# Optimization experiments

Hardware: AMD Instinct MI355X
Metric: run time of the kernel (lower is better)

## Reference

```python
import jax, jax.numpy as jnp
import numpy as np
from jax import lax

B_, CIN, COUT, H, W = 8, 64, 64, 64, 64
DIN, DSTATE, K, DTRANK = 128, 16, 4, 4  # d_inner=2*C, d_state=16, 4 scan dirs, dt_rank=ceil(64/16)


def setup_inputs():
    key = jax.random.key(0)
    ks = jax.random.split(key, 10)
    f = lambda k, s, sc=0.02: jax.random.normal(k, s, jnp.float32) * sc
    return {
        "x": jax.random.normal(ks[0], (B_, CIN, H, W), jnp.float32),
        "conv_w": f(ks[1], (COUT, CIN, 3, 3)),
        "conv_b": jnp.zeros((COUT,), jnp.float32),
        "gn_g": jnp.ones((COUT,), jnp.float32),
        "gn_b": jnp.zeros((COUT,), jnp.float32),
        "ln1_g": jnp.ones((COUT,), jnp.float32),
        "ln1_b": jnp.zeros((COUT,), jnp.float32),
        "in_proj_w": f(ks[2], (COUT, 2 * DIN)),
        "dw_w": f(ks[3], (DIN, 1, 3, 3)),
        "dw_b": jnp.zeros((DIN,), jnp.float32),
        "x_proj_w": f(ks[4], (K, DTRANK + 2 * DSTATE, DIN)),
        "dt_w": f(ks[5], (K, DIN, DTRANK)),
        "dt_b": f(ks[6], (K, DIN), 0.01),
        "A_logs": jnp.tile(jnp.log(jnp.arange(1, DSTATE + 1, dtype=jnp.float32)), (K, DIN, 1)),
        "Ds": jnp.ones((K, DIN), jnp.float32),
        "out_norm_g": jnp.ones((DIN,), jnp.float32),
        "out_norm_b": jnp.zeros((DIN,), jnp.float32),
        "out_proj_w": f(ks[7], (DIN, COUT)),
    }


def _ln(x, g, b, eps=1e-5):
    m = x.mean(-1, keepdims=True)
    v = ((x - m) ** 2).mean(-1, keepdims=True)
    return (x - m) * lax.rsqrt(v + eps) * g + b


def reference(x, conv_w, conv_b, gn_g, gn_b, ln1_g, ln1_b, in_proj_w, dw_w, dw_b,
              x_proj_w, dt_w, dt_b, A_logs, Ds, out_norm_g, out_norm_b, out_proj_w):
    # BasicConv2d: conv3x3 (stride 1, pad 1) + GroupNorm(2) + SiLU
    y = lax.conv_general_dilated(x, conv_w, (1, 1), [(1, 1), (1, 1)],
                                 dimension_numbers=("NCHW", "OIHW", "NCHW"))
    y = y + conv_b[None, :, None, None]
    Bb, C, Hh, Ww = y.shape
    yg = y.reshape(Bb, 2, C // 2, Hh, Ww)
    m = yg.mean((2, 3, 4), keepdims=True)
    v = ((yg - m) ** 2).mean((2, 3, 4), keepdims=True)
    y = ((yg - m) * lax.rsqrt(v + 1e-5)).reshape(Bb, C, Hh, Ww)
    y = y * gn_g[None, :, None, None] + gn_b[None, :, None, None]
    y = jax.nn.silu(y)
    # VSSBlock on NHWC: LN -> SS2D -> residual
    xb = y.transpose(0, 2, 3, 1)                       # (B,H,W,C)
    h = _ln(xb, ln1_g, ln1_b)
    xz = h @ in_proj_w                                 # (B,H,W,2*DIN)
    xm, z = jnp.split(xz, 2, axis=-1)
    xm = xm.transpose(0, 3, 1, 2)                      # (B,DIN,H,W)
    xm = lax.conv_general_dilated(xm, dw_w, (1, 1), [(1, 1), (1, 1)],
                                  dimension_numbers=("NCHW", "OIHW", "NCHW"),
                                  feature_group_count=DIN)
    xm = jax.nn.silu(xm + dw_b[None, :, None, None])
    L = Hh * Ww
    x1 = xm.reshape(Bb, DIN, L)                        # HW order
    x2 = xm.transpose(0, 1, 3, 2).reshape(Bb, DIN, L)  # WH order
    xs = jnp.stack([x1, x2], 1)
    xs = jnp.concatenate([xs, jnp.flip(xs, -1)], 1)    # (B,4,DIN,L)
    xdbl = jnp.einsum("bkdl,kcd->bkcl", xs, x_proj_w)
    dts, Bs, Cs = jnp.split(xdbl, [DTRANK, DTRANK + DSTATE], axis=2)
    dts = jnp.einsum("bkrl,kdr->bkdl", dts, dt_w)
    dt = jax.nn.softplus(dts + dt_b[None, :, :, None])  # (B,4,DIN,L)
    A = -jnp.exp(A_logs)                                # (K,DIN,DSTATE)
    # selective scan over L (time-major)
    u_t = xs.transpose(3, 0, 1, 2)
    dt_t = dt.transpose(3, 0, 1, 2)
    B_t = Bs.transpose(3, 0, 1, 2)
    C_t = Cs.transpose(3, 0, 1, 2)

    def step(hst, inp):
        u, d, Bc, Cc = inp
        hst = hst * jnp.exp(d[..., None] * A) + (d * u)[..., None] * Bc[:, :, None, :]
        return hst, jnp.einsum("bkdn,bkn->bkd", hst, Cc)

    h0 = jnp.zeros((Bb, K, DIN, DSTATE), xs.dtype)
    _, ys = lax.scan(step, h0, (u_t, dt_t, B_t, C_t))  # ys: (L,B,4,DIN)
    out_y = ys.transpose(1, 2, 3, 0) + Ds[None, :, :, None] * xs
    inv_y = jnp.flip(out_y[:, 2:4], -1)
    wh_y = out_y[:, 1].reshape(Bb, DIN, Ww, Hh).transpose(0, 1, 3, 2).reshape(Bb, DIN, L)
    invwh_y = inv_y[:, 1].reshape(Bb, DIN, Ww, Hh).transpose(0, 1, 3, 2).reshape(Bb, DIN, L)
    yv = out_y[:, 0] + inv_y[:, 0] + wh_y + invwh_y    # (B,DIN,L)
    yv = yv.transpose(0, 2, 1).reshape(Bb, Hh, Ww, DIN)
    yv = _ln(yv, out_norm_g, out_norm_b)
    yv = yv * jax.nn.silu(z)
    vss = xb + yv @ out_proj_w                          # VSSBlock residual
    return vss.transpose(0, 3, 1, 2) + y                # MambaDU residual
```

## Files before the change

kernel.cpp:

```cpp
#include <hip/hip_runtime.h>
#include <hip/hip_bf16.h>

#define BD   8
#define CD   64
#define HD   64
#define WD   64
#define LD   4096
#define DINN 128
#define KDIR 4
#define NST  16
#define SUBL 32
#define L2E  1.442695040888963f

typedef const float* fp;

__device__ __forceinline__ float sigm(float x) { return 1.f / (1.f + __expf(-x)); }
__device__ __forceinline__ float softplusf(float x) {
    float e = __expf(-fabsf(x));
    return fmaxf(x, 0.f) + __logf(1.f + e);
}
__device__ __forceinline__ int pmap(int k, int l) {
    int m = (k & 2) ? (LD - 1 - l) : l;
    return (k & 1) ? (((m & 63) << 6) | (m >> 6)) : m;
}

__global__ __launch_bounds__(256) void k_conv(fp x, fp cw, fp cb, float* conv_out, float* gstats) {
    __shared__ float xt[64][3][68];
    __shared__ float red[4][4];
    int bx = blockIdx.x; int b = bx >> 6; int h = bx & 63;
    int t = threadIdx.x;
    for (int idx = t; idx < 64 * 3 * 64; idx += 256) {
        int ci = idx / 192, rem = idx % 192, r = rem >> 6, w = rem & 63;
        int hs = h + r - 1;
        float v = 0.f;
        if (hs >= 0 && hs < 64) v = x[((b * 64 + ci) * 64 + hs) * 64 + w];
        xt[ci][r][w + 1] = v;
    }
    for (int idx = t; idx < 64 * 3; idx += 256) {
        int ci = idx / 3, r = idx % 3;
        xt[ci][r][0] = 0.f; xt[ci][r][65] = 0.f; xt[ci][r][66] = 0.f; xt[ci][r][67] = 0.f;
    }
    __syncthreads();
    int co = t & 63, wq = t >> 6;
    float acc[16];
#pragma unroll
    for (int j = 0; j < 16; j++) acc[j] = 0.f;
    for (int ci = 0; ci < 64; ci++) {
        float wv[9];
        fp wp = cw + (co * 64 + ci) * 9;
#pragma unroll
        for (int q = 0; q < 9; q++) wv[q] = wp[q];
#pragma unroll
        for (int r = 0; r < 3; r++) {
            const float* row = &xt[ci][r][wq * 16];
            float xw[20];
#pragma unroll
            for (int q = 0; q < 5; q++) {
                float4 f = ((const float4*)row)[q];
                xw[4 * q] = f.x; xw[4 * q + 1] = f.y; xw[4 * q + 2] = f.z; xw[4 * q + 3] = f.w;
            }
#pragma unroll
            for (int j = 0; j < 16; j++)
                acc[j] += wv[r * 3 + 0] * xw[j] + wv[r * 3 + 1] * xw[j + 1] + wv[r * 3 + 2] * xw[j + 2];
        }
    }
    float bias = cb[co];
    __syncthreads();
    float* ot = &xt[0][0][0];
#pragma unroll
    for (int j = 0; j < 16; j++) ot[co * 64 + wq * 16 + j] = acc[j] + bias;
    __syncthreads();
    float ps0 = 0.f, pq0 = 0.f, ps1 = 0.f, pq1 = 0.f;
    for (int idx = t; idx < 4096; idx += 256) {
        int c2 = idx >> 6, w2 = idx & 63;
        float v = ot[idx];
        conv_out[((b * 64 + c2) * 64 + h) * 64 + w2] = v;
        bool g0 = c2 < 32;
        float v2 = v * v;
        ps0 += g0 ? v : 0.f; pq0 += g0 ? v2 : 0.f;
        ps1 += g0 ? 0.f : v; pq1 += g0 ? 0.f : v2;
    }
#pragma unroll
    for (int off = 32; off; off >>= 1) {
        ps0 += __shfl_xor(ps0, off); pq0 += __shfl_xor(pq0, off);
        ps1 += __shfl_xor(ps1, off); pq1 += __shfl_xor(pq1, off);
    }
    int wid = t >> 6;
    if ((t & 63) == 0) { red[wid][0] = ps0; red[wid][1] = pq0; red[wid][2] = ps1; red[wid][3] = pq1; }
    __syncthreads();
    if (t < 4) {
        float v = red[0][t] + red[1][t] + red[2][t] + red[3][t];
        atomicAdd(&gstats[b * 4 + t], v);
    }
}

__global__ __launch_bounds__(256) void k_gnapply(const float* conv_out, const float* gstats,
                                                 fp gng, fp gnb, float* y_nhwc) {
    __shared__ float tile[64][65];
    int bx = blockIdx.x; int b = bx >> 6; int p0 = (bx & 63) * 64;
    int t = threadIdx.x;
    const float invN = 1.f / (32.f * 4096.f);
    float s0 = gstats[b * 4 + 0], q0 = gstats[b * 4 + 1];
    float s1 = gstats[b * 4 + 2], q1 = gstats[b * 4 + 3];
    float m0 = s0 * invN, r0 = rsqrtf(q0 * invN - m0 * m0 + 1e-5f);
    float m1 = s1 * invN, r1 = rsqrtf(q1 * invN - m1 * m1 + 1e-5f);
    for (int idx = t; idx < 4096; idx += 256) {
        int c = idx >> 6, pi = idx & 63;
        float v = conv_out[(b * 64 + c) * LD + p0 + pi];
        float mean = (c < 32) ? m0 : m1, rstd = (c < 32) ? r0 : r1;
        v = (v - mean) * rstd * gng[c] + gnb[c];
        v = v * sigm(v);
        tile[c][pi] = v;
    }
    __syncthreads();
    for (int idx = t; idx < 4096; idx += 256) {
        int pi = idx >> 6, c = idx & 63;
        y_nhwc[(b * LD + p0 + pi) * 64 + c] = tile[c][pi];
    }
}

__global__ __launch_bounds__(256) void k_lninproj(const float* y_nhwc, fp lng, fp lnb, fp ipw,
                                                  float* xmc, float* zsil) {
    __shared__ float hn[4][64];
    int bp0 = blockIdx.x * 4;
    int t = threadIdx.x;
    int pix = t >> 6, lane = t & 63;
    {
        float v = y_nhwc[(bp0 + pix) * 64 + lane];
        float s = v, s2 = v * v;
#pragma unroll
        for (int off = 32; off; off >>= 1) { s += __shfl_xor(s, off); s2 += __shfl_xor(s2, off); }
        float mean = s * (1.f / 64.f);
        float rstd = rsqrtf(s2 * (1.f / 64.f) - mean * mean + 1e-5f);
        hn[pix][lane] = (v - mean) * rstd * lng[lane] + lnb[lane];
    }
    __syncthreads();
    float a0 = 0.f, a1 = 0.f, a2 = 0.f, a3 = 0.f;
    for (int c = 0; c < 64; c++) {
        float w = ipw[c * 256 + t];
        a0 += hn[0][c] * w; a1 += hn[1][c] * w; a2 += hn[2][c] * w; a3 += hn[3][c] * w;
    }
    float accv[4] = {a0, a1, a2, a3};
#pragma unroll
    for (int p = 0; p < 4; p++) {
        int bp = bp0 + p;
        float v = accv[p];
        if (t < 128) xmc[bp * 128 + t] = v;
        else         zsil[bp * 128 + (t - 128)] = v * sigm(v);
    }
}

__global__ __launch_bounds__(256) void k_dwconv(const float* xmc, fp dww, fp dwb, float* xm_dw) {
    int id = blockIdx.x * 256 + threadIdx.x;
    int d = id & 127, p = (id >> 7) & (LD - 1), b = id >> 19;
    int h = p >> 6, w = p & 63;
    float wv[9];
#pragma unroll
    for (int q = 0; q < 9; q++) wv[q] = dww[d * 9 + q];
    float acc = dwb[d];
#pragma unroll
    for (int i = 0; i < 3; i++) {
        int hs = h + i - 1; if (hs < 0 || hs > 63) continue;
#pragma unroll
        for (int j = 0; j < 3; j++) {
            int ws = w + j - 1; if (ws < 0 || ws > 63) continue;
            acc += xmc[((b << 12) + (hs << 6) + ws) * 128 + d] * wv[i * 3 + j];
        }
    }
    acc = acc * sigm(acc);
    xm_dw[id] = acc;
}

__global__ __launch_bounds__(192) void k_proj(const float* xm_dw, fp xpw, float* dts4, float* xBC) {
    __shared__ float u_lds[64 * 130];
    __shared__ float w_lds[128 * 40];
    int bx = blockIdx.x;
    int lt = bx & 63; int bk = bx >> 6; int k = bk & 3; int b = bk >> 2;
    int l0 = lt * 64;
    int t = threadIdx.x;
    for (int idx = t; idx < 36 * 128; idx += 192) {
        int c = idx % 36, d = idx / 36;
        w_lds[d * 40 + c] = xpw[(k * 36 + c) * 128 + d];
    }
    for (int idx = t; idx < 64 * 128; idx += 192) {
        int l = idx >> 7, d = idx & 127;
        u_lds[l * 130 + d] = xm_dw[(b * LD + pmap(k, l0 + l)) * 128 + d];
    }
    __syncthreads();
    int l = t & 63, cg = t >> 6;
    float acc[12];
#pragma unroll
    for (int i = 0; i < 12; i++) acc[i] = 0.f;
    for (int d = 0; d < 128; d++) {
        float uv = u_lds[l * 130 + d];
        const float* wr = &w_lds[d * 40 + cg * 12];
#pragma unroll
        for (int q = 0; q < 3; q++) {
            float4 f = ((const float4*)wr)[q];
            acc[4 * q + 0] += f.x * uv;
            acc[4 * q + 1] += f.y * uv;
            acc[4 * q + 2] += f.z * uv;
            acc[4 * q + 3] += f.w * uv;
        }
    }
    int base = bk * LD + l0 + l;
#pragma unroll
    for (int i = 0; i < 12; i++) {
        int c = cg * 12 + i;
        if (c < 4) dts4[base * 4 + c] = acc[i];
        else       xBC[base * 32 + (c - 4)] = acc[i];
    }
}

__global__ __launch_bounds__(256) void k_scan1(const float* xm_dw, const float* dts4, const float* xBC,
                                               fp dtw, fp dtbp, fp alog,
                                               float* Pbuf, float* Hbuf, int NCr, int CLr) {
    __shared__ float s_dt[SUBL * 128];
    __shared__ float s_b[SUBL * 16];
    __shared__ float s_d4[SUBL * 4];
    int c = blockIdx.x, k = blockIdx.y, b = blockIdx.z;
    int t = threadIdx.x; int d = t & 127; int ng = t >> 7;
    int bk = b * 4 + k;
    int kd = k * 128 + d;
    float w0 = dtw[kd * 4 + 0], w1 = dtw[kd * 4 + 1], w2 = dtw[kd * 4 + 2], w3 = dtw[kd * 4 + 3];
    float dtb = dtbp[kd];
    float base = -__expf(alog[kd * 16]) * L2E;
    float A2[8];
    bool geo = true;
#pragma unroll
    for (int n = 0; n < 8; n++) {
        A2[n] = -__expf(alog[kd * 16 + ng * 8 + n]) * L2E;
        float ideal = (float)(ng * 8 + n + 1) * base;
        geo = geo && (fabsf(A2[n] - ideal) <= 1e-4f * fabsf(ideal));
    }
    float h[8]; float sdt = 0.f;
#pragma unroll
    for (int n = 0; n < 8; n++) h[n] = 0.f;
    int l0 = c * CLr;
    for (int ss = 0; ss < CLr; ss += SUBL) {
        int ls = l0 + ss;
        const float4* gd = (const float4*)&dts4[(size_t)(bk * LD + ls) * 4];
        if (t < SUBL) ((float4*)s_d4)[t] = gd[t];
        const float4* gx = (const float4*)&xBC[(size_t)(bk * LD + ls) * 32];
        for (int i = t; i < SUBL * 4; i += 256) { int s = i >> 2, q = i & 3; ((float4*)s_b)[s * 4 + q] = gx[s * 8 + q]; }
        __syncthreads();
#pragma unroll
        for (int i = 0; i < SUBL / 2; i++) {
            int s = (t >> 7) + i * 2;
            float4 dv = ((const float4*)s_d4)[s];
            s_dt[s * 128 + d] = softplusf(dv.x * w0 + dv.y * w1 + dv.z * w2 + dv.w * w3 + dtb);
        }
        __syncthreads();
        int pbase = pmap(k, ls);
        int pstep = pmap(k, ls + 1) - pbase;
        const float* up = xm_dw + (size_t)(b * LD + pbase) * 128 + d;
        long ustep = (long)pstep * 128;
        if (geo) {
#pragma unroll 2
            for (int s = 0; s < SUBL; s++) {
                float dtv = s_dt[s * 128 + d];
                sdt += dtv;
                float r = exp2f(dtv * base);
                float u = *up; up += ustep;
                float du = dtv * u;
                const float4* Bp = (const float4*)&s_b[s * 16 + ng * 8];
                float4 B0 = Bp[0], B1 = Bp[1];
                float r2 = r * r, r3 = r2 * r, r4 = r2 * r2;
                float p5 = r4 * r, p6 = r4 * r2, p7 = r4 * r3, p8 = r4 * r4;
                float a1 = r, a2 = r2, a3 = r3, a4 = r4, a5 = p5, a6 = p6, a7 = p7, a8 = p8;
                if (ng == 1) { a1 *= p8; a2 *= p8; a3 *= p8; a4 *= p8; a5 *= p8; a6 *= p8; a7 *= p8; a8 *= p8; }
                h[0] = a1 * h[0] + du * B0.x;
                h[1] = a2 * h[1] + du * B0.y;
                h[2] = a3 * h[2] + du * B0.z;
                h[3] = a4 * h[3] + du * B0.w;
                h[4] = a5 * h[4] + du * B1.x;
                h[5] = a6 * h[5] + du * B1.y;
                h[6] = a7 * h[6] + du * B1.z;
                h[7] = a8 * h[7] + du * B1.w;
            }
        } else {
#pragma unroll 2
            for (int s = 0; s < SUBL; s++) {
                float dtv = s_dt[s * 128 + d];
                sdt += dtv;
                float u = *up; up += ustep;
                float du = dtv * u;
                const float4* Bp = (const float4*)&s_b[s * 16 + ng * 8];
                float4 B0 = Bp[0], B1 = Bp[1];
                float Bv[8] = {B0.x, B0.y, B0.z, B0.w, B1.x, B1.y, B1.z, B1.w};
#pragma unroll
                for (int n = 0; n < 8; n++) {
                    float a = exp2f(dtv * A2[n]);
                    h[n] = a * h[n] + du * Bv[n];
                }
            }
        }
        __syncthreads();
    }
    int obase = (bk * NCr + c) * 2048 + ng * 8 * 128 + d;
#pragma unroll
    for (int n = 0; n < 8; n++) {
        Pbuf[obase + n * 128] = exp2f(sdt * A2[n]);
        Hbuf[obase + n * 128] = h[n];
    }
}

__global__ __launch_bounds__(256) void k_scan2(const float* Pbuf, const float* Hbuf, float* Hinit, int NCr) {
    int id = blockIdx.x * 256 + threadIdx.x;
    int nd = id & 2047; int bk = id >> 11;
    float h = 0.f;
    int base = bk * NCr * 2048 + nd;
    for (int c = 0; c < NCr; c++) {
        int idx = base + c * 2048;
        Hinit[idx] = h;
        h = Hbuf[idx] + Pbuf[idx] * h;
    }
}

__global__ __launch_bounds__(256) void k_scan3(const float* xm_dw, const float* dts4, const float* xBC,
                                               fp dtw, fp dtbp, fp alog, fp dsp,
                                               const float* Hinit, float* yv, int NCr, int CLr) {
    __shared__ float s_dt[SUBL * 128];
    __shared__ float s_bc[SUBL * 32];
    __shared__ float s_d4[SUBL * 4];
    int c = blockIdx.x, k = blockIdx.y, b = blockIdx.z;
    int t = threadIdx.x; int d = t & 127; int ng = t >> 7;
    int bk = b * 4 + k;
    int kd = k * 128 + d;
    float w0 = dtw[kd * 4 + 0], w1 = dtw[kd * 4 + 1], w2 = dtw[kd * 4 + 2], w3 = dtw[kd * 4 + 3];
    float dtb = dtbp[kd];
    float Dv = dsp[kd];
    float base = -__expf(alog[kd * 16]) * L2E;
    float A2[8];
    bool geo = true;
#pragma unroll
    for (int n = 0; n < 8; n++) {
        A2[n] = -__expf(alog[kd * 16 + ng * 8 + n]) * L2E;
        float ideal = (float)(ng * 8 + n + 1) * base;
        geo = geo && (fabsf(A2[n] - ideal) <= 1e-4f * fabsf(ideal));
    }
    int hbase = (bk * NCr + c) * 2048 + ng * 8 * 128 + d;
    float h[8];
#pragma unroll
    for (int n = 0; n < 8; n++) h[n] = Hinit[hbase + n * 128];
    int l0 = c * CLr;
    for (int ss = 0; ss < CLr; ss += SUBL) {
        int ls = l0 + ss;
        const float4* gd = (const float4*)&dts4[(size_t)(bk * LD + ls) * 4];
        if (t < SUBL) ((float4*)s_d4)[t] = gd[t];
        const float4* gx = (const float4*)&xBC[(size_t)(bk * LD + ls) * 32];
        ((float4*)s_bc)[t] = gx[t];
        __syncthreads();
#pragma unroll
        for (int i = 0; i < SUBL / 2; i++) {
            int s = (t >> 7) + i * 2;
            float4 dv = ((const float4*)s_d4)[s];
            s_dt[s * 128 + d] = softplusf(dv.x * w0 + dv.y * w1 + dv.z * w2 + dv.w * w3 + dtb);
        }
        __syncthreads();
        int pbase = pmap(k, ls);
        int pstep = pmap(k, ls + 1) - pbase;
        const float* up = xm_dw + (size_t)(b * LD + pbase) * 128 + d;
        float* yp = yv + (size_t)(b * LD + pbase) * 128 + d;
        long ustep = (long)pstep * 128;
        if (geo) {
#pragma unroll 2
            for (int s = 0; s < SUBL; s++) {
                float dtv = s_dt[s * 128 + d];
                float r = exp2f(dtv * base);
                float u = *up; up += ustep;
                float du = dtv * u;
                const float4* Bp = (const float4*)&s_bc[s * 32 + ng * 8];
                float4 B0 = Bp[0], B1 = Bp[1];
                const float4* Cp = (const float4*)&s_bc[s * 32 + 16 + ng * 8];
                float4 C0 = Cp[0], C1 = Cp[1];
                float r2 = r * r, r3 = r2 * r, r4 = r2 * r2;
                float p5 = r4 * r, p6 = r4 * r2, p7 = r4 * r3, p8 = r4 * r4;
                float a1 = r, a2 = r2, a3 = r3, a4 = r4, a5 = p5, a6 = p6, a7 = p7, a8 = p8;
                if (ng == 1) { a1 *= p8; a2 *= p8; a3 *= p8; a4 *= p8; a5 *= p8; a6 *= p8; a7 *= p8; a8 *= p8; }
                float y;
                h[0] = a1 * h[0] + du * B0.x; y  = h[0] * C0.x;
                h[1] = a2 * h[1] + du * B0.y; y += h[1] * C0.y;
                h[2] = a3 * h[2] + du * B0.z; y += h[2] * C0.z;
                h[3] = a4 * h[3] + du * B0.w; y += h[3] * C0.w;
                h[4] = a5 * h[4] + du * B1.x; y += h[4] * C1.x;
                h[5] = a6 * h[5] + du * B1.y; y += h[5] * C1.y;
                h[6] = a7 * h[6] + du * B1.z; y += h[6] * C1.z;
                h[7] = a8 * h[7] + du * B1.w; y += h[7] * C1.w;
                if (ng == 0) y += Dv * u;
                atomicAdd(yp, y); yp += ustep;
            }
        } else {
#pragma unroll 2
            for (int s = 0; s < SUBL; s++) {
                float dtv = s_dt[s * 128 + d];
                float u = *up; up += ustep;
                float du = dtv * u;
                const float4* Bp = (const float4*)&s_bc[s * 32 + ng * 8];
                float4 B0 = Bp[0], B1 = Bp[1];
                const float4* Cp = (const float4*)&s_bc[s * 32 + 16 + ng * 8];
                float4 C0 = Cp[0], C1 = Cp[1];
                float Bv[8] = {B0.x, B0.y, B0.z, B0.w, B1.x, B1.y, B1.z, B1.w};
                float Cv[8] = {C0.x, C0.y, C0.z, C0.w, C1.x, C1.y, C1.z, C1.w};
                float y = 0.f;
#pragma unroll
                for (int n = 0; n < 8; n++) {
                    float a = exp2f(dtv * A2[n]);
                    h[n] = a * h[n] + du * Bv[n];
                    y += h[n] * Cv[n];
                }
                if (ng == 0) y += Dv * u;
                atomicAdd(yp, y); yp += ustep;
            }
        }
        __syncthreads();
    }
}

__global__ __launch_bounds__(256) void k_final(const float* yv, const float* zsil, const float* y_nhwc,
                                               fp ong, fp onb, fp opw, float* out) {
    __shared__ float ylds[2][128];
    __shared__ float red[2][2][2];
    __shared__ float part[2][2][64];
    int bp0 = blockIdx.x * 2;
    int t = threadIdx.x;
    int pix = t >> 7, tl = t & 127;
    int bp = bp0 + pix;
    float v = yv[bp * 128 + tl];
    float s = v, s2 = v * v;
#pragma unroll
    for (int off = 32; off; off >>= 1) { s += __shfl_xor(s, off); s2 += __shfl_xor(s2, off); }
    int wh = (t >> 6) & 1;
    if ((t & 63) == 0) { red[pix][wh][0] = s; red[pix][wh][1] = s2; }
    __syncthreads();
    float S = red[pix][0][0] + red[pix][1][0], S2 = red[pix][0][1] + red[pix][1][1];
    float mean = S * (1.f / 128.f);
    float rstd = rsqrtf(S2 * (1.f / 128.f) - mean * mean + 1e-5f);
    float vn = (v - mean) * rstd * ong[tl] + onb[tl];
    vn *= zsil[bp * 128 + tl];
    ylds[pix][tl] = vn;
    __syncthreads();
    {
        int px = t >> 7, half = (t >> 6) & 1, co = t & 63;
        float acc = 0.f;
        const float* yrow = &ylds[px][half * 64];
        const float* wcol = &opw[half * 64 * 64 + co];
#pragma unroll 16
        for (int dd = 0; dd < 64; dd++) acc += yrow[dd] * wcol[dd * 64];
        part[px][half][co] = acc;
    }
    __syncthreads();
    if (t < 128) {
        int pp = t >> 6, co = t & 63;
        int bpo = bp0 + pp;
        float a = part[pp][0][co] + part[pp][1][co];
        float yb = y_nhwc[bpo * 64 + co];
        out[((bpo >> 12) * 64 + co) * LD + (bpo & 4095)] = 2.f * yb + a;
    }
}

extern "C" void kernel_launch(void* const* d_in, const int* in_sizes, int n_in,
                              void* d_out, int out_size, void* d_ws, size_t ws_size,
                              hipStream_t stream) {
    fp x    = (fp)d_in[0];
    fp cw   = (fp)d_in[1];
    fp cb   = (fp)d_in[2];
    fp gng  = (fp)d_in[3];
    fp gnb  = (fp)d_in[4];
    fp lng  = (fp)d_in[5];
    fp lnb  = (fp)d_in[6];
    fp ipw  = (fp)d_in[7];
    fp dww  = (fp)d_in[8];
    fp dwb  = (fp)d_in[9];
    fp xpw  = (fp)d_in[10];
    fp dtw  = (fp)d_in[11];
    fp dtb  = (fp)d_in[12];
    fp alog = (fp)d_in[13];
    fp dsp  = (fp)d_in[14];
    fp ong  = (fp)d_in[15];
    fp onb  = (fp)d_in[16];
    fp opw  = (fp)d_in[17];

    float* w = (float*)d_ws;
    float* conv_out = w;  w += BD * 64 * LD;
    float* y_nhwc   = w;  w += BD * LD * 64;
    float* gstats   = w;  w += 32;
    float* xmc      = w;  w += BD * LD * 128;
    float* zsil     = w;  w += BD * LD * 128;
    float* xm_dw    = w;  w += BD * LD * 128;
    float* dts4     = w;  w += BD * KDIR * LD * 4;
    float* xBC      = w;  w += BD * KDIR * LD * 32;
    float* yv       = w;  w += BD * LD * 128;
    size_t base_floats = (size_t)(w - (float*)d_ws);

    int NCr = 32;
    size_t perbuf64 = (size_t)32 * 64 * 2048;
    float *Pbuf, *Hbuf, *Hinit;
    if (ws_size >= (base_floats + 3 * perbuf64) * sizeof(float)) {
        NCr = 64;
        Pbuf  = w;  w += perbuf64;
        Hbuf  = w;  w += perbuf64;
        Hinit = w;  w += perbuf64;
    } else {
        Pbuf  = xmc;
        Hbuf  = xmc + (size_t)32 * 32 * 2048;
        Hinit = conv_out;
    }
    int CLr = LD / NCr;
    if (ws_size < base_floats * sizeof(float)) return;

    hipMemsetAsync(gstats, 0, 32 * sizeof(float), stream);
    k_conv<<<BD * HD, 256, 0, stream>>>(x, cw, cb, conv_out, gstats);
    k_gnapply<<<BD * 64, 256, 0, stream>>>(conv_out, gstats, gng, gnb, y_nhwc);
    k_lninproj<<<BD * LD / 4, 256, 0, stream>>>(y_nhwc, lng, lnb, ipw, xmc, zsil);
    k_dwconv<<<BD * LD * 128 / 256, 256, 0, stream>>>(xmc, dww, dwb, xm_dw);
    k_proj<<<BD * KDIR * 64, 192, 0, stream>>>(xm_dw, xpw, dts4, xBC);
    k_scan1<<<dim3(NCr, KDIR, BD), 256, 0, stream>>>(xm_dw, dts4, xBC, dtw, dtb, alog, Pbuf, Hbuf, NCr, CLr);
    k_scan2<<<256, 256, 0, stream>>>(Pbuf, Hbuf, Hinit, NCr);
    hipMemsetAsync(yv, 0, (size_t)BD * LD * 128 * sizeof(float), stream);
    k_scan3<<<dim3(NCr, KDIR, BD), 256, 0, stream>>>(xm_dw, dts4, xBC, dtw, dtb, alog, dsp, Hinit, yv, NCr, CLr);
    k_final<<<BD * LD / 2, 256, 0, stream>>>(yv, zsil, y_nhwc, ong, onb, opw, (float*)d_out);
}
```

Measured before the change: 514.7 us.

## Give each scan thread all 16 states and recompute softplus inline

The chunked scan kernels now use 128 threads per block, with each thread owning all 16 state dimensions for one channel. Previously two thread groups split the states 8/8. This halves the atomicAdd traffic to yv in scan3 and drops the redundant u loads and dt computation. The separate shared-memory softplus pass and one barrier per sub-chunk are removed, with dt recomputed inline per step, and the sub-chunk size grows from 32 to 64. The trade-off is fewer threads per chunk, more registers per thread, and a longer serial dependency chain in each thread.

```diff
diff --git a/kernel.cpp b/kernel.cpp
--- a/kernel.cpp
+++ b/kernel.cpp
@@ -9,7 +9,6 @@
 #define DINN 128
 #define KDIR 4
 #define NST  16
-#define SUBL 32
 #define L2E  1.442695040888963f
 
 typedef const float* fp;
@@ -212,94 +211,86 @@
     }
 }
 
-__global__ __launch_bounds__(256) void k_scan1(const float* xm_dw, const float* dts4, const float* xBC,
+__global__ __launch_bounds__(128) void k_scan1(const float* xm_dw, const float* dts4, const float* xBC,
                                                fp dtw, fp dtbp, fp alog,
                                                float* Pbuf, float* Hbuf, int NCr, int CLr) {
-    __shared__ float s_dt[SUBL * 128];
-    __shared__ float s_b[SUBL * 16];
-    __shared__ float s_d4[SUBL * 4];
+    __shared__ float s_b[64 * 16];
+    __shared__ float s_d4[64 * 4];
     int c = blockIdx.x, k = blockIdx.y, b = blockIdx.z;
-    int t = threadIdx.x; int d = t & 127; int ng = t >> 7;
+    int d = threadIdx.x;
     int bk = b * 4 + k;
     int kd = k * 128 + d;
     float w0 = dtw[kd * 4 + 0], w1 = dtw[kd * 4 + 1], w2 = dtw[kd * 4 + 2], w3 = dtw[kd * 4 + 3];
     float dtb = dtbp[kd];
     float base = -__expf(alog[kd * 16]) * L2E;
-    float A2[8];
+    float A2[16];
     bool geo = true;
 #pragma unroll
-    for (int n = 0; n < 8; n++) {
-        A2[n] = -__expf(alog[kd * 16 + ng * 8 + n]) * L2E;
-        float ideal = (float)(ng * 8 + n + 1) * base;
+    for (int n = 0; n < 16; n++) {
+        A2[n] = -__expf(alog[kd * 16 + n]) * L2E;
+        float ideal = (float)(n + 1) * base;
         geo = geo && (fabsf(A2[n] - ideal) <= 1e-4f * fabsf(ideal));
     }
-    float h[8]; float sdt = 0.f;
-#pragma unroll
-    for (int n = 0; n < 8; n++) h[n] = 0.f;
+    float h[16]; float sdt = 0.f;
+#pragma unroll
+    for (int n = 0; n < 16; n++) h[n] = 0.f;
     int l0 = c * CLr;
-    for (int ss = 0; ss < CLr; ss += SUBL) {
+    for (int ss = 0; ss < CLr; ss += 64) {
+        if (ss) __syncthreads();
         int ls = l0 + ss;
         const float4* gd = (const float4*)&dts4[(size_t)(bk * LD + ls) * 4];
-        if (t < SUBL) ((float4*)s_d4)[t] = gd[t];
+        if (d < 64) ((float4*)s_d4)[d] = gd[d];
         const float4* gx = (const float4*)&xBC[(size_t)(bk * LD + ls) * 32];
-        for (int i = t; i < SUBL * 4; i += 256) { int s = i >> 2, q = i & 3; ((float4*)s_b)[s * 4 + q] = gx[s * 8 + q]; }
-        __syncthreads();
-#pragma unroll
-        for (int i = 0; i < SUBL / 2; i++) {
-            int s = (t >> 7) + i * 2;
-            float4 dv = ((const float4*)s_d4)[s];
-            s_dt[s * 128 + d] = softplusf(dv.x * w0 + dv.y * w1 + dv.z * w2 + dv.w * w3 + dtb);
-        }
+        for (int i = d; i < 64 * 4; i += 128) { int s = i >> 2, q = i & 3; ((float4*)s_b)[i] = gx[s * 8 + q]; }
         __syncthreads();
         int pbase = pmap(k, ls);
         int pstep = pmap(k, ls + 1) - pbase;
         const float* up = xm_dw + (size_t)(b * LD + pbase) * 128 + d;
         long ustep = (long)pstep * 128;
         if (geo) {
-#pragma unroll 2
-            for (int s = 0; s < SUBL; s++) {
-                float dtv = s_dt[s * 128 + d];
+#pragma unroll 4
+            for (int s = 0; s < 64; s++) {
+                float4 dv = ((const float4*)s_d4)[s];
+                float dtv = softplusf(dv.x * w0 + dv.y * w1 + dv.z * w2 + dv.w * w3 + dtb);
                 sdt += dtv;
-                float r = exp2f(dtv * base);
                 float u = *up; up += ustep;
                 float du = dtv * u;
-                const float4* Bp = (const float4*)&s_b[s * 16 + ng * 8];
-                float4 B0 = Bp[0], B1 = Bp[1];
+                const float4* Bp = (const float4*)&s_b[s * 16];
+                float4 B0 = Bp[0], B1 = Bp[1], B2 = Bp[2], B3 = Bp[3];
+                float r = exp2f(dtv * base);
                 float r2 = r * r, r3 = r2 * r, r4 = r2 * r2;
-                float p5 = r4 * r, p6 = r4 * r2, p7 = r4 * r3, p8 = r4 * r4;
-                float a1 = r, a2 = r2, a3 = r3, a4 = r4, a5 = p5, a6 = p6, a7 = p7, a8 = p8;
-                if (ng == 1) { a1 *= p8; a2 *= p8; a3 *= p8; a4 *= p8; a5 *= p8; a6 *= p8; a7 *= p8; a8 *= p8; }
-                h[0] = a1 * h[0] + du * B0.x;
-                h[1] = a2 * h[1] + du * B0.y;
-                h[2] = a3 * h[2] + du * B0.z;
-                h[3] = a4 * h[3] + du * B0.w;
-                h[4] = a5 * h[4] + du * B1.x;
-                h[5] = a6 * h[5] + du * B1.y;
-                h[6] = a7 * h[6] + du * B1.z;
-                h[7] = a8 * h[7] + du * B1.w;
+                float r5 = r4 * r, r6 = r4 * r2, r7 = r4 * r3, r8 = r4 * r4;
+                float r9 = r8 * r, r10 = r8 * r2, r11 = r8 * r3, r12 = r8 * r4;
+                float r13 = r8 * r5, r14 = r8 * r6, r15 = r8 * r7, r16 = r8 * r8;
+                h[0]  = r   * h[0]  + du * B0.x;  h[1]  = r2  * h[1]  + du * B0.y;
+                h[2]  = r3  * h[2]  + du * B0.z;  h[3]  = r4  * h[3]  + du * B0.w;
+                h[4]  = r5  * h[4]  + du * B1.x;  h[5]  = r6  * h[5]  + du * B1.y;
+                h[6]  = r7  * h[6]  + du * B1.z;  h[7]  = r8  * h[7]  + du * B1.w;
+                h[8]  = r9  * h[8]  + du * B2.x;  h[9]  = r10 * h[9]  + du * B2.y;
+                h[10] = r11 * h[10] + du * B2.z;  h[11] = r12 * h[11] + du * B2.w;
+                h[12] = r13 * h[12] + du * B3.x;  h[13] = r14 * h[13] + du * B3.y;
+                h[14] = r15 * h[14] + du * B3.z;  h[15] = r16 * h[15] + du * B3.w;
             }
         } else {
 #pragma unroll 2
-            for (int s = 0; s < SUBL; s++) {
-                float dtv = s_dt[s * 128 + d];
+            for (int s = 0; s < 64; s++) {
+                float4 dv = ((const float4*)s_d4)[s];
+                float dtv = softplusf(dv.x * w0 + dv.y * w1 + dv.z * w2 + dv.w * w3 + dtb);
                 sdt += dtv;
                 float u = *up; up += ustep;
                 float du = dtv * u;
-                const float4* Bp = (const float4*)&s_b[s * 16 + ng * 8];
-                float4 B0 = Bp[0], B1 = Bp[1];
-                float Bv[8] = {B0.x, B0.y, B0.z, B0.w, B1.x, B1.y, B1.z, B1.w};
-#pragma unroll
-                for (int n = 0; n < 8; n++) {
+                const float* Bp = &s_b[s * 16];
+#pragma unroll
+                for (int n = 0; n < 16; n++) {
                     float a = exp2f(dtv * A2[n]);
-                    h[n] = a * h[n] + du * Bv[n];
+                    h[n] = a * h[n] + du * Bp[n];
                 }
             }
         }
-        __syncthreads();
-    }
-    int obase = (bk * NCr + c) * 2048 + ng * 8 * 128 + d;
-#pragma unroll
-    for (int n = 0; n < 8; n++) {
+    }
+    int obase = (bk * NCr + c) * 2048 + d;
+#pragma unroll
+    for (int n = 0; n < 16; n++) {
         Pbuf[obase + n * 128] = exp2f(sdt * A2[n]);
         Hbuf[obase + n * 128] = h[n];
     }
@@ -317,46 +308,39 @@
     }
 }
 
-__global__ __launch_bounds__(256) void k_scan3(const float* xm_dw, const float* dts4, const float* xBC,
+__global__ __launch_bounds__(128) void k_scan3(const float* xm_dw, const float* dts4, const float* xBC,
                                                fp dtw, fp dtbp, fp alog, fp dsp,
                                                const float* Hinit, float* yv, int NCr, int CLr) {
-    __shared__ float s_dt[SUBL * 128];
-    __shared__ float s_bc[SUBL * 32];
-    __shared__ float s_d4[SUBL * 4];
+    __shared__ float s_bc[64 * 32];
+    __shared__ float s_d4[64 * 4];
     int c = blockIdx.x, k = blockIdx.y, b = blockIdx.z;
-    int t = threadIdx.x; int d = t & 127; int ng = t >> 7;
+    int d = threadIdx.x;
     int bk = b * 4 + k;
     int kd = k * 128 + d;
     float w0 = dtw[kd * 4 + 0], w1 = dtw[kd * 4 + 1], w2 = dtw[kd * 4 + 2], w3 = dtw[kd * 4 + 3];
     float dtb = dtbp[kd];
     float Dv = dsp[kd];
     float base = -__expf(alog[kd * 16]) * L2E;
-    float A2[8];
+    float A2[16];
     bool geo = true;
 #pragma unroll
-    for (int n = 0; n < 8; n++) {
-        A2[n] = -__expf(alog[kd * 16 + ng * 8 + n]) * L2E;
-        float ideal = (float)(ng * 8 + n + 1) * base;
+    for (int n = 0; n < 16; n++) {
+        A2[n] = -__expf(alog[kd * 16 + n]) * L2E;
+        float ideal = (float)(n + 1) * base;
         geo = geo && (fabsf(A2[n] - ideal) <= 1e-4f * fabsf(ideal));
     }
-    int hbase = (bk * NCr + c) * 2048 + ng * 8 * 128 + d;
-    float h[8];
-#pragma unroll
-    for (int n = 0; n < 8; n++) h[n] = Hinit[hbase + n * 128];
+    int hbase = (bk * NCr + c) * 2048 + d;
+    float h[16];
+#pragma unroll
+    for (int n = 0; n < 16; n++) h[n] = Hinit[hbase + n * 128];
     int l0 = c * CLr;
-    for (int ss = 0; ss < CLr; ss += SUBL) {
+    for (int ss = 0; ss < CLr; ss += 64) {
+        if (ss) __syncthreads();
         int ls = l0 + ss;
         const float4* gd = (const float4*)&dts4[(size_t)(bk * LD + ls) * 4];
-        if (t < SUBL) ((float4*)s_d4)[t] = gd[t];
+        if (d < 64) ((float4*)s_d4)[d] = gd[d];
         const float4* gx = (const float4*)&xBC[(size_t)(bk * LD + ls) * 32];
-        ((float4*)s_bc)[t] = gx[t];
-        __syncthreads();
-#pragma unroll
-        for (int i = 0; i < SUBL / 2; i++) {
-            int s = (t >> 7) + i * 2;
-            float4 dv = ((const float4*)s_d4)[s];
-            s_dt[s * 128 + d] = softplusf(dv.x * w0 + dv.y * w1 + dv.z * w2 + dv.w * w3 + dtb);
-        }
+        for (int i = d; i < 64 * 8; i += 128) ((float4*)s_bc)[i] = gx[i];
         __syncthreads();
         int pbase = pmap(k, ls);
         int pstep = pmap(k, ls + 1) - pbase;
@@ -364,56 +348,59 @@
         float* yp = yv + (size_t)(b * LD + pbase) * 128 + d;
         long ustep = (long)pstep * 128;
         if (geo) {
-#pragma unroll 2
-            for (int s = 0; s < SUBL; s++) {
-                float dtv = s_dt[s * 128 + d];
-                float r = exp2f(dtv * base);
+#pragma unroll 4
+            for (int s = 0; s < 64; s++) {
+                float4 dv = ((const float4*)s_d4)[s];
+                float dtv = softplusf(dv.x * w0 + dv.y * w1 + dv.z * w2 + dv.w * w3 + dtb);
                 float u = *up; up += ustep;
                 float du = dtv * u;
-                const float4* Bp = (const float4*)&s_bc[s * 32 + ng * 8];
-                float4 B0 = Bp[0], B1 = Bp[1];
-                const float4* Cp = (const float4*)&s_bc[s * 32 + 16 + ng * 8];
-                float4 C0 = Cp[0], C1 = Cp[1];
+                const float4* Bp = (const float4*)&s_bc[s * 32];
+                float4 B0 = Bp[0], B1 = Bp[1], B2 = Bp[2], B3 = Bp[3];
+                float4 C0 = Bp[4], C1 = Bp[5], C2 = Bp[6], C3 = Bp[7];
+                float r = exp2f(dtv * base);
                 float r2 = r * r, r3 = r2 * r, r4 = r2 * r2;
-                float p5 = r4 * r, p6 = r4 * r2, p7 = r4 * r3, p8 = r4 * r4;
-                float a1 = r, a2 = r2, a3 = r3, a4 = r4, a5 = p5, a6 = p6, a7 = p7, a8 = p8;
-                if (ng == 1) { a1 *= p8; a2 *= p8; a3 *= p8; a4 *= p8; a5 *= p8; a6 *= p8; a7 *= p8; a8 *= p8; }
+                float r5 = r4 * r, r6 = r4 * r2, r7 = r4 * r3, r8 = r4 * r4;
+                float r9 = r8 * r, r10 = r8 * r2, r11 = r8 * r3, r12 = r8 * r4;
+                float r13 = r8 * r5, r14 = r8 * r6, r15 = r8 * r7, r16 = r8 * r8;
                 float y;
-                h[0] = a1 * h[0] + du * B0.x; y  = h[0] * C0.x;
-                h[1] = a2 * h[1] + du * B0.y; y += h[1] * C0.y;
-                h[2] = a3 * h[2] + du * B0.z; y += h[2] * C0.z;
-                h[3] = a4 * h[3] + du * B0.w; y += h[3] * C0.w;
-                h[4] = a5 * h[4] + du * B1.x; y += h[4] * C1.x;
-                h[5] = a6 * h[5] + du * B1.y; y += h[5] * C1.y;
-                h[6] = a7 * h[6] + du * B1.z; y += h[6] * C1.z;
-                h[7] = a8 * h[7] + du * B1.w; y += h[7] * C1.w;
-                if (ng == 0) y += Dv * u;
+                h[0]  = r   * h[0]  + du * B0.x;  y  = h[0]  * C0.x;
+                h[1]  = r2  * h[1]  + du * B0.y;  y += h[1]  * C0.y;
+                h[2]  = r3  * h[2]  + du * B0.z;  y += h[2]  * C0.z;
+                h[3]  = r4  * h[3]  + du * B0.w;  y += h[3]  * C0.w;
+                h[4]  = r5  * h[4]  + du * B1.x;  y += h[4]  * C1.x;
+                h[5]  = r6  * h[5]  + du * B1.y;  y += h[5]  * C1.y;
+                h[6]  = r7  * h[6]  + du * B1.z;  y += h[6]  * C1.z;
+                h[7]  = r8  * h[7]  + du * B1.w;  y += h[7]  * C1.w;
+                h[8]  = r9  * h[8]  + du * B2.x;  y += h[8]  * C2.x;
+                h[9]  = r10 * h[9]  + du * B2.y;  y += h[9]  * C2.y;
+                h[10] = r11 * h[10] + du * B2.z;  y += h[10] * C2.z;
+                h[11] = r12 * h[11] + du * B2.w;  y += h[11] * C2.w;
+                h[12] = r13 * h[12] + du * B3.x;  y += h[12] * C3.x;
+                h[13] = r14 * h[13] + du * B3.y;  y += h[13] * C3.y;
+                h[14] = r15 * h[14] + du * B3.z;  y += h[14] * C3.z;
+                h[15] = r16 * h[15] + du * B3.w;  y += h[15] * C3.w;
+                y += Dv * u;
                 atomicAdd(yp, y); yp += ustep;
             }
         } else {
 #pragma unroll 2
-            for (int s = 0; s < SUBL; s++) {
-                float dtv = s_dt[s * 128 + d];
+            for (int s = 0; s < 64; s++) {
+                float4 dv = ((const float4*)s_d4)[s];
+                float dtv = softplusf(dv.x * w0 + dv.y * w1 + dv.z * w2 + dv.w * w3 + dtb);
                 float u = *up; up += ustep;
                 float du = dtv * u;
-                const float4* Bp = (const float4*)&s_bc[s * 32 + ng * 8];
-                float4 B0 = Bp[0], B1 = Bp[1];
-                const float4* Cp = (const float4*)&s_bc[s * 32 + 16 + ng * 8];
-                float4 C0 = Cp[0], C1 = Cp[1];
-                float Bv[8] = {B0.x, B0.y, B0.z, B0.w, B1.x, B1.y, B1.z, B1.w};
-                float Cv[8] = {C0.x, C0.y, C0.z, C0.w, C1.x, C1.y, C1.z, C1.w};
+                const float* Bp = &s_bc[s * 32];
                 float y = 0.f;
 #pragma unroll
-                for (int n = 0; n < 8; n++) {
+                for (int n = 0; n < 16; n++) {
                     float a = exp2f(dtv * A2[n]);
-                    h[n] = a * h[n] + du * Bv[n];
-                    y += h[n] * Cv[n];
+                    h[n] = a * h[n] + du * Bp[n];
+                    y += h[n] * Bp[16 + n];
                 }
-                if (ng == 0) y += Dv * u;
+                y += Dv * u;
                 atomicAdd(yp, y); yp += ustep;
             }
         }
-        __syncthreads();
     }
 }
 
@@ -515,9 +502,9 @@
     k_lninproj<<<BD * LD / 4, 256, 0, stream>>>(y_nhwc, lng, lnb, ipw, xmc, zsil);
     k_dwconv<<<BD * LD * 128 / 256, 256, 0, stream>>>(xmc, dww, dwb, xm_dw);
     k_proj<<<BD * KDIR * 64, 192, 0, stream>>>(xm_dw, xpw, dts4, xBC);
-    k_scan1<<<dim3(NCr, KDIR, BD), 256, 0, stream>>>(xm_dw, dts4, xBC, dtw, dtb, alog, Pbuf, Hbuf, NCr, CLr);
+    k_scan1<<<dim3(NCr, KDIR, BD), 128, 0, stream>>>(xm_dw, dts4, xBC, dtw, dtb, alog, Pbuf, Hbuf, NCr, CLr);
     k_scan2<<<256, 256, 0, stream>>>(Pbuf, Hbuf, Hinit, NCr);
     hipMemsetAsync(yv, 0, (size_t)BD * LD * 128 * sizeof(float), stream);
-    k_scan3<<<dim3(NCr, KDIR, BD), 256, 0, stream>>>(xm_dw, dts4, xBC, dtw, dtb, alog, dsp, Hinit, yv, NCr, CLr);
+    k_scan3<<<dim3(NCr, KDIR, BD), 128, 0, stream>>>(xm_dw, dts4, xBC, dtw, dtb, alog, dsp, Hinit, yv, NCr, CLr);
     k_final<<<BD * LD / 2, 256, 0, stream>>>(yv, zsil, y_nhwc, ong, onb, opw, (float*)d_out);
 }
```

New measurement: 447.4 us. 1.15x faster.
